# Kernel optimization log

Hardware: AMD Instinct MI355X
Metric: run time of the kernel (lower is better)

The kernel has to match this reference:

```python
import jax, jax.numpy as jnp
import numpy as np

B, C, H, W = 32, 512, 32, 32
N = H * W            # seq_len = 1024
HEADS = 8
DH = C // HEADS      # 64
K = 256              # linformer low-rank
EPS = 1e-5


def setup_inputs() -> dict:
    key = jax.random.key(0)
    ks = jax.random.split(key, 10)
    s = 0.02
    return {
        "x": jax.random.normal(ks[0], (B, C, H, W), dtype=jnp.float32),
        "pos": jax.random.normal(ks[1], (1, N, C), dtype=jnp.float32),
        "ln_g": jnp.ones((C,), dtype=jnp.float32),
        "ln_b": jnp.zeros((C,), dtype=jnp.float32),
        "Wq": jax.random.normal(ks[2], (C, C), dtype=jnp.float32) * s,
        "Wk": jax.random.normal(ks[3], (C, C), dtype=jnp.float32) * s,
        "Wv": jax.random.normal(ks[4], (C, C), dtype=jnp.float32) * s,
        "proj_k": jax.random.normal(ks[5], (N, K), dtype=jnp.float32) * s,
        "proj_v": jax.random.normal(ks[6], (N, K), dtype=jnp.float32) * s,
        "Wo": jax.random.normal(ks[7], (C, C), dtype=jnp.float32) * s,
        "bo": jnp.zeros((C,), dtype=jnp.float32),
    }


def reference(x, pos, ln_g, ln_b, Wq, Wk, Wv, proj_k, proj_v, Wo, bo):
    b, c, h, w = x.shape
    n = h * w
    # b c h w -> b (h w) c
    xf = x.reshape(b, c, n).transpose(0, 2, 1) + pos
    # LayerNorm (biased variance, eps=1e-5) + ReLU; dropout = identity (eval)
    mu = xf.mean(-1, keepdims=True)
    var = jnp.var(xf, axis=-1, keepdims=True)
    y = (xf - mu) * jax.lax.rsqrt(var + EPS) * ln_g + ln_b
    y = jax.nn.relu(y)
    # Linformer self-attention
    q = y @ Wq                                   # [b,n,c]
    k_ = jnp.einsum('bnd,nk->bkd', y @ Wk, proj_k)  # [b,K,c]
    v_ = jnp.einsum('bnd,nk->bkd', y @ Wv, proj_v)  # [b,K,c]
    q = q.reshape(b, n, HEADS, DH)
    k_ = k_.reshape(b, K, HEADS, DH)
    v_ = v_.reshape(b, K, HEADS, DH)
    dots = jnp.einsum('bnhd,bkhd->bhnk', q, k_) * (DH ** -0.5)
    attn = jax.nn.softmax(dots, axis=-1)
    out = jnp.einsum('bhnk,bkhd->bnhd', attn, v_).reshape(b, n, c)
    out = out @ Wo + bo
    # residual with (x + pos), then back to b c h w
    out = out + xf
    return out.transpose(0, 2, 1).reshape(b, c, h, w)
```

## Files before the change

kernel.cpp:

```cpp
#include <hip/hip_runtime.h>
#include <hip/hip_bf16.h>
#include <cstdint>

#define BB  32
#define CC  512
#define NN  1024
#define HH  8
#define DHH 64
#define KR  256

using f32x4  = __attribute__((ext_vector_type(4))) float;
using f32x16 = __attribute__((ext_vector_type(16))) float;
using bf16x8 = __attribute__((ext_vector_type(8))) __bf16;
using u32x4  = __attribute__((ext_vector_type(4))) unsigned int;

__device__ __forceinline__ unsigned short f2bf(float f) {
  unsigned int u = __float_as_uint(f);
  u += 0x7fffu + ((u >> 16) & 1u);
  return (unsigned short)(u >> 16);
}

__device__ __forceinline__ float bf2f(unsigned short u) {
  return __uint_as_float(((unsigned int)u) << 16);
}

__device__ __forceinline__ unsigned int pknat(float a, float b) {
  unsigned short ua = __builtin_bit_cast(unsigned short, (__bf16)a);
  unsigned short ub = __builtin_bit_cast(unsigned short, (__bf16)b);
  return (unsigned int)ua | ((unsigned int)ub << 16);
}

__device__ __forceinline__ void gload16(const void* gsrc, void* ldst) {
  __builtin_amdgcn_global_load_lds(
      (const __attribute__((address_space(1))) unsigned int*)gsrc,
      (__attribute__((address_space(3))) unsigned int*)ldst, 16, 0, 0);
}

__global__ __launch_bounds__(256) void transcvt_all(
    const float* __restrict__ w0, const float* __restrict__ w1,
    const float* __restrict__ w2, const float* __restrict__ w3,
    const float* __restrict__ p0, const float* __restrict__ p1,
    const float* __restrict__ pos,
    unsigned short* __restrict__ d0, unsigned short* __restrict__ d1,
    unsigned short* __restrict__ d2, unsigned short* __restrict__ d3,
    unsigned short* __restrict__ e0, unsigned short* __restrict__ e1,
    float* __restrict__ posT) {
  const int m = blockIdx.y;
  int idx = blockIdx.x * 256 + threadIdx.x;
  if (m == 6) {
    #pragma unroll
    for (int h = 0; h < 2; ++h) {
      int e = idx + h * 262144;
      int c = e >> 10, n = e & 1023;
      posT[e] = pos[(size_t)n * CC + c];
    }
    return;
  }
  const float* src = m==0?w0:m==1?w1:m==2?w2:m==3?w3:m==4?p0:p1;
  unsigned short* dst = m==0?d0:m==1?d1:m==2?d2:m==3?d3:m==4?e0:e1;
  if (m < 4) {
    int dr = idx & 511;
    int dc = idx >> 9;
    dst[idx] = f2bf(src[(size_t)dr * 512 + dc]);
  } else {
    int n = idx & 1023, kk = idx >> 10;
    dst[idx] = f2bf(src[(size_t)n * 256 + kk]);
  }
}

__global__ __launch_bounds__(1024) void ln_relu_kernel(
    const float* __restrict__ x, const float* __restrict__ posT,
    const float* __restrict__ g, const float* __restrict__ bta,
    unsigned short* __restrict__ y, unsigned short* __restrict__ yT) {
  __shared__ unsigned short tile[512][68];
  __shared__ float smp[16][16][8];
  __shared__ float smu[64], srs[64];
  const int b = blockIdx.y, n0 = blockIdx.x * 64;
  const int tid = threadIdx.x;
  const int wv = tid >> 6, ln_ = tid & 63;
  const int q = tid & 15;
  const int rr = tid >> 4;
  const int t4 = q * 4;
  const float* xb = x    + (size_t)b * CC * NN + n0;
  const float* pb = posT + n0;

  float s[4] = {0.f,0.f,0.f,0.f}, s2[4] = {0.f,0.f,0.f,0.f};
  #pragma unroll
  for (int half = 0; half < 2; ++half) {
    float4 xv[4], pv[4];
    #pragma unroll
    for (int i = 0; i < 4; ++i) {
      const int c = (half * 4 + i) * 64 + rr;
      xv[i] = *reinterpret_cast<const float4*>(&xb[(size_t)c * NN + t4]);
      pv[i] = *reinterpret_cast<const float4*>(&pb[(size_t)c * NN + t4]);
    }
    #pragma unroll
    for (int i = 0; i < 4; ++i) {
      const int c = (half * 4 + i) * 64 + rr;
      float f0 = xv[i].x + pv[i].x, f1 = xv[i].y + pv[i].y;
      float f2 = xv[i].z + pv[i].z, f3 = xv[i].w + pv[i].w;
      s[0] += f0; s2[0] += f0 * f0;
      s[1] += f1; s2[1] += f1 * f1;
      s[2] += f2; s2[2] += f2 * f2;
      s[3] += f3; s2[3] += f3 * f3;
      uint2 w; w.x = pknat(f0, f1); w.y = pknat(f2, f3);
      *reinterpret_cast<uint2*>(&tile[c][t4]) = w;
    }
  }
  #pragma unroll
  for (int d = 16; d < 64; d <<= 1)
    #pragma unroll
    for (int k = 0; k < 4; ++k) {
      s[k]  += __shfl_xor(s[k],  d, 64);
      s2[k] += __shfl_xor(s2[k], d, 64);
    }
  if (ln_ < 16) {
    #pragma unroll
    for (int k = 0; k < 4; ++k) {
      smp[wv][ln_][k]     = s[k];
      smp[wv][ln_][k + 4] = s2[k];
    }
  }
  __syncthreads();

  if (tid < 64) {
    const int qq = tid >> 2, k = tid & 3;
    float ss = 0.f, ss2 = 0.f;
    #pragma unroll
    for (int w = 0; w < 16; ++w) { ss += smp[w][qq][k]; ss2 += smp[w][qq][k + 4]; }
    float mu = ss * (1.f / 512.f);
    float var = ss2 * (1.f / 512.f) - mu * mu;
    smu[tid] = mu;
    srs[tid] = rsqrtf(var + 1e-5f);
  }
  __syncthreads();

  {
    const int cq = tid & 127;
    const int c0 = cq * 4;
    const float4 gv = *reinterpret_cast<const float4*>(&g[c0]);
    const float4 bv = *reinterpret_cast<const float4*>(&bta[c0]);
    #pragma unroll
    for (int it = 0; it < 8; ++it) {
      const int tok = it * 8 + (tid >> 7);
      const float mu = smu[tok], rs = srs[tok];
      float o0 = (bf2f(tile[c0 + 0][tok]) - mu) * rs * gv.x + bv.x;
      float o1 = (bf2f(tile[c0 + 1][tok]) - mu) * rs * gv.y + bv.y;
      float o2 = (bf2f(tile[c0 + 2][tok]) - mu) * rs * gv.z + bv.z;
      float o3 = (bf2f(tile[c0 + 3][tok]) - mu) * rs * gv.w + bv.w;
      o0 = o0 > 0.f ? o0 : 0.f;
      o1 = o1 > 0.f ? o1 : 0.f;
      o2 = o2 > 0.f ? o2 : 0.f;
      o3 = o3 > 0.f ? o3 : 0.f;
      unsigned short b0 = f2bf(o0), b1 = f2bf(o1), b2 = f2bf(o2), b3 = f2bf(o3);
      uint2 u; u.x = (unsigned int)b0 | ((unsigned int)b1 << 16);
      u.y = (unsigned int)b2 | ((unsigned int)b3 << 16);
      *reinterpret_cast<uint2*>(&y[((size_t)b * NN + n0 + tok) * CC + c0]) = u;
      tile[c0 + 0][tok] = b0; tile[c0 + 1][tok] = b1;
      tile[c0 + 2][tok] = b2; tile[c0 + 3][tok] = b3;
    }
  }
  __syncthreads();

  {
    const int c = tid & 511, hf = tid >> 9;
    const int toff = hf * 32;
    unsigned short* ytb = yT + (size_t)b * CC * NN + (size_t)c * NN + n0 + toff;
    #pragma unroll
    for (int v4 = 0; v4 < 4; ++v4) {
      uint2 a0 = *reinterpret_cast<const uint2*>(&tile[c][toff + v4 * 8]);
      uint2 a1 = *reinterpret_cast<const uint2*>(&tile[c][toff + v4 * 8 + 4]);
      uint4 w; w.x = a0.x; w.y = a0.y; w.z = a1.x; w.w = a1.y;
      *reinterpret_cast<uint4*>(&ytb[v4 * 8]) = w;
    }
  }
}

template <int MODE>
__global__ __launch_bounds__(256) void gemm_tn(
    const unsigned short* __restrict__ A, int lda, long long strideA,
    const unsigned short* __restrict__ Bt, int ldb, long long strideB,
    unsigned short* __restrict__ Cb, long long strideC,
    unsigned short* __restrict__ Cb2, long long strideC2,
    int Nn, int Kk, int TB,
    const float* __restrict__ xres, const float* __restrict__ posT,
    const float* __restrict__ bias, float* __restrict__ outF) {
  __shared__ __align__(16) unsigned short sh[24576];
  unsigned short* aL = sh;
  unsigned short* bL = sh + 12288;
  const int zb = blockIdx.z;
  int sel = 0, mb;
  if (MODE == 3) {
    sel = blockIdx.y >> 1;
    mb = ((blockIdx.y & 1) + sel * 2) * 128;
    if (sel == 1) Bt += (size_t)512 * 512;
  } else {
    mb = blockIdx.y * 128;
  }
  const int nb = blockIdx.x * 128;
  A  += (size_t)strideA * zb;
  Bt += (size_t)strideB * zb;
  Cb += (size_t)strideC * zb;
  if (MODE == 3) Cb2 += (size_t)strideC2 * zb;
  const int tid  = threadIdx.x;
  const int lane = tid & 63;
  const int wave = tid >> 6;
  const int wm = (wave >> 1) * 64, wn = (wave & 1) * 64;
  const int sr  = lane >> 2;
  const int scw = lane & 3;
  f32x4 acc[4][4] = {};

  auto stage = [&](int buf, int k0) {
    #pragma unroll
    for (int i = 0; i < 2; ++i) {
      int rbase = wave * 32 + i * 16;
      int row = rbase + sr;
      int ca = scw ^ ((row ^ (row >> 2)) & 3);
      gload16(&A [(size_t)(mb + row) * lda + k0 + ca * 8], &aL[buf * 4096 + rbase * 32]);
      gload16(&Bt[(size_t)(nb + row) * ldb + k0 + ca * 8], &bL[buf * 4096 + rbase * 32]);
    }
  };

  const int nt = Kk >> 5;
  stage(0, 0);
  stage(1, 32);
  asm volatile("s_waitcnt vmcnt(4)" ::: "memory");
  __builtin_amdgcn_s_barrier();
  __builtin_amdgcn_sched_barrier(0);

  int cbuf = 0;
  for (int t = 0; t < nt; ++t) {
    if (t + 2 < nt) stage(cbuf == 0 ? 2 : cbuf - 1, (t + 2) << 5);

    bf16x8 af[4], bfv[4];
    const int kc = lane >> 4;
    #pragma unroll
    for (int i = 0; i < 4; ++i) {
      int ra = wm + i * 16 + (lane & 15);
      int rb = wn + i * 16 + (lane & 15);
      af[i]  = *reinterpret_cast<const bf16x8*>(&aL[cbuf * 4096 + ra * 32 + (kc ^ ((ra ^ (ra >> 2)) & 3)) * 8]);
      bfv[i] = *reinterpret_cast<const bf16x8*>(&bL[cbuf * 4096 + rb * 32 + (kc ^ ((rb ^ (rb >> 2)) & 3)) * 8]);
    }
    #pragma unroll
    for (int i = 0; i < 4; ++i)
      #pragma unroll
      for (int j = 0; j < 4; ++j)
        acc[i][j] = __builtin_amdgcn_mfma_f32_16x16x32_bf16(af[i], bfv[j], acc[i][j], 0, 0, 0);

    if (t + 2 < nt)      { asm volatile("s_waitcnt vmcnt(4)" ::: "memory"); }
    else if (t + 1 < nt) { asm volatile("s_waitcnt vmcnt(0)" ::: "memory"); }
    if (t + 1 < nt) {
      __builtin_amdgcn_s_barrier();
      __builtin_amdgcn_sched_barrier(0);
    }
    cbuf = (cbuf == 2) ? 0 : cbuf + 1;
  }

  if (MODE == 2) {
    float* Ct = reinterpret_cast<float*>(sh);
    const int halfsel = wave >> 1;
    const int t0base = nb & 1023;
    const int bcell = nb >> 10;
    #pragma unroll
    for (int half = 0; half < 2; ++half) {
      __syncthreads();
      if (halfsel == half) {
        #pragma unroll
        for (int i = 0; i < 4; ++i) {
          int rloc = i * 16 + ((lane >> 4) << 2);
          #pragma unroll
          for (int j = 0; j < 4; ++j) {
            int cl = wn + j * 16 + (lane & 15);
            #pragma unroll
            for (int t = 0; t < 4; ++t)
              Ct[(rloc + t) * 132 + cl] = acc[i][j][t];
          }
        }
      }
      __syncthreads();
      #pragma unroll
      for (int p8 = 0; p8 < 8; ++p8) {
        int e = p8 * 256 + tid;
        int r = e >> 5, f4 = (e & 31) * 4;
        int c = mb + half * 64 + r;
        size_t base = ((size_t)bcell * CC + c) * NN + t0base + f4;
        float4 cv = *reinterpret_cast<const float4*>(&Ct[r * 132 + f4]);
        float4 xv = *reinterpret_cast<const float4*>(&xres[base]);
        float4 pv = *reinterpret_cast<const float4*>(&posT[(size_t)c * NN + t0base + f4]);
        float bc = bias[c];
        float4 ov;
        ov.x = cv.x + xv.x + pv.x + bc;
        ov.y = cv.y + xv.y + pv.y + bc;
        ov.z = cv.z + xv.z + pv.z + bc;
        ov.w = cv.w + xv.w + pv.w + bc;
        *reinterpret_cast<float4*>(&outF[base]) = ov;
      }
    }
  } else {
    const bool transp = (MODE == 1) || (MODE == 3 && sel == 1);
    auto Ct = (unsigned short (*)[136])sh;
    __syncthreads();
    #pragma unroll
    for (int i = 0; i < 4; ++i) {
      const int r0 = wm + i * 16 + ((lane >> 4) << 2);
      #pragma unroll
      for (int j = 0; j < 4; ++j) {
        const int cl = wn + j * 16 + (lane & 15);
        #pragma unroll
        for (int t = 0; t < 4; ++t) {
          if (!transp) Ct[r0 + t][cl] = f2bf(acc[i][j][t]);
          else         Ct[cl][r0 + t] = f2bf(acc[i][j][t]);
        }
      }
    }
    __syncthreads();
    const int rr = tid >> 4, ch = tid & 15;
    #pragma unroll
    for (int it = 0; it < 8; ++it) {
      const int r = it * 16 + rr;
      uint4 v = *reinterpret_cast<const uint4*>(&Ct[r][ch * 8]);
      if (!transp)
        *reinterpret_cast<uint4*>(&Cb[(size_t)(mb + r) * Nn + nb + ch * 8]) = v;
      else if (MODE == 1)
        *reinterpret_cast<uint4*>(&Cb[(size_t)(nb + r) * TB + mb + ch * 8]) = v;
      else
        *reinterpret_cast<uint4*>(&Cb2[(size_t)(nb + r) * TB + (mb - 256) + ch * 8]) = v;
    }
  }
}

__global__ __launch_bounds__(256, 2) void attn_kernel(
    const unsigned short* __restrict__ q,
    const unsigned short* __restrict__ kB,
    const unsigned short* __restrict__ vT,
    unsigned short* __restrict__ O) {
  __shared__ __align__(16) unsigned short smem[32768];
  const int wgid = blockIdx.x;
  const int grp  = wgid & 255;
  const int tg   = wgid >> 8;
  const int h = grp & 7, b = grp >> 3;
  const int wave = threadIdx.x >> 6, lane = threadIdx.x & 63;
  const int t32 = lane & 31, g2 = lane >> 5;
  const int tokb = tg * 128 + wave * 32;

  const unsigned short* qp = q + ((size_t)(b * NN + tokb + t32)) * CC + h * DHH + g2 * 8;
  bf16x8 qf[4];
  #pragma unroll
  for (int st = 0; st < 4; ++st)
    qf[st] = *reinterpret_cast<const bf16x8*>(qp + (size_t)st * 16);

  {
    const unsigned short* kb = kB + ((size_t)b * KR) * CC + h * DHH;
    const int r0w = wave * 64;
    #pragma unroll
    for (int i = 0; i < 8; ++i) {
      int row = r0w + i * 8 + (lane >> 3);
      int sc  = (lane & 7) ^ (row & 7);
      gload16(kb + (size_t)row * CC + sc * 8, &smem[(r0w + i * 8) * 64]);
    }
    const unsigned short* vb = vT + ((size_t)b * CC + h * DHH) * KR;
    const int v0w = wave * 16;
    #pragma unroll
    for (int i = 0; i < 8; ++i) {
      int row = v0w + i * 2 + (lane >> 5);
      int sc  = (lane & 31) ^ (row & 7);
      gload16(vb + (size_t)row * KR + sc * 8, &smem[16384 + (v0w + i * 2) * 256]);
    }
  }
  __syncthreads();

  f32x16 s8[8] = {};
  #pragma unroll
  for (int t8 = 0; t8 < 8; ++t8) {
    const int row = t8 * 32 + t32;
    #pragma unroll
    for (int st = 0; st < 4; ++st) {
      int ch = (2 * st + g2) ^ (row & 7);
      bf16x8 kf = *reinterpret_cast<const bf16x8*>(&smem[row * 64 + ch * 8]);
      s8[t8] = __builtin_amdgcn_mfma_f32_32x32x16_bf16(kf, qf[st], s8[t8], 0, 0, 0);
    }
  }

  float m = -1e30f;
  #pragma unroll
  for (int t8 = 0; t8 < 8; ++t8)
    #pragma unroll
    for (int r = 0; r < 16; ++r) m = fmaxf(m, s8[t8][r]);
  m = fmaxf(m, __shfl_xor(m, 32));
  const float cexp = 0.125f * 1.44269504088896f;
  float ls = 0.f;
  #pragma unroll
  for (int t8 = 0; t8 < 8; ++t8)
    #pragma unroll
    for (int r = 0; r < 16; ++r) {
      float p = __builtin_amdgcn_exp2f((s8[t8][r] - m) * cexp);
      s8[t8][r] = p;
      ls += p;
    }
  ls += __shfl_xor(ls, 32);
  float rinv = __builtin_amdgcn_rcpf(ls);

  f32x16 o0 = {}, o1 = {};
  #pragma unroll
  for (int t8 = 0; t8 < 8; ++t8) {
    unsigned int pkd[8];
    #pragma unroll
    for (int qq = 0; qq < 4; ++qq) {
      pkd[qq * 2 + 0] = pknat(s8[t8][4 * qq + 0], s8[t8][4 * qq + 1]);
      pkd[qq * 2 + 1] = pknat(s8[t8][4 * qq + 2], s8[t8][4 * qq + 3]);
    }
    #pragma unroll
    for (int a = 0; a < 2; ++a) {
      const int ks = t8 * 2 + a;
      unsigned int xe0 = pkd[4 * a + 0], xe1 = pkd[4 * a + 1];
      unsigned int xo0 = pkd[4 * a + 2], xo1 = pkd[4 * a + 3];
      unsigned int d0 = g2 ? __shfl_xor(xo0, 32) : xe0;
      unsigned int d1 = g2 ? __shfl_xor(xo1, 32) : xe1;
      unsigned int d2 = g2 ? xo0 : __shfl_xor(xe0, 32);
      unsigned int d3 = g2 ? xo1 : __shfl_xor(xe1, 32);
      u32x4 pv_ = {d0, d1, d2, d3};
      bf16x8 pa = __builtin_bit_cast(bf16x8, pv_);
      #pragma unroll
      for (int dt = 0; dt < 2; ++dt) {
        int row = dt * 32 + t32;
        int ch = (2 * ks + g2) ^ (row & 7);
        bf16x8 bv = *reinterpret_cast<const bf16x8*>(&smem[16384 + row * 256 + ch * 8]);
        if (dt == 0) o0 = __builtin_amdgcn_mfma_f32_32x32x16_bf16(pa, bv, o0, 0, 0, 0);
        else         o1 = __builtin_amdgcn_mfma_f32_32x32x16_bf16(pa, bv, o1, 0, 0, 0);
      }
    }
  }

  unsigned short* Ob = O + ((size_t)(b * NN + tokb)) * CC + h * DHH;
  #pragma unroll
  for (int r = 0; r < 16; ++r) {
    int tl = (r & 3) + 8 * (r >> 2) + 4 * g2;
    float rs = __shfl(rinv, tl);
    Ob[(size_t)tl * CC + t32]      = f2bf(o0[r] * rs);
    Ob[(size_t)tl * CC + 32 + t32] = f2bf(o1[r] * rs);
  }
}

extern "C" void kernel_launch(void* const* d_in, const int* in_sizes, int n_in,
                              void* d_out, int out_size, void* d_ws, size_t ws_size,
                              hipStream_t stream) {
  const float* x    = (const float*)d_in[0];
  const float* pos  = (const float*)d_in[1];
  const float* ln_g = (const float*)d_in[2];
  const float* ln_b = (const float*)d_in[3];
  const float* Wq   = (const float*)d_in[4];
  const float* Wk   = (const float*)d_in[5];
  const float* Wv   = (const float*)d_in[6];
  const float* pk   = (const float*)d_in[7];
  const float* pv   = (const float*)d_in[8];
  const float* Wo   = (const float*)d_in[9];
  const float* bo   = (const float*)d_in[10];
  float* out = (float*)d_out;

  unsigned short* ws = (unsigned short*)d_ws;
  size_t off = 0;
  auto alloc = [&](size_t elems) { unsigned short* p = ws + off; off += elems; return p; };
  unsigned short* WqT     = alloc(512 * 512);
  unsigned short* WkT     = alloc(512 * 512);
  unsigned short* WvT     = alloc(512 * 512);
  unsigned short* WoT     = alloc(512 * 512);
  unsigned short* projcat = alloc((size_t)512 * 1024);
  float*          posTb   = (float*)alloc((size_t)512 * 1024 * 2);
  unsigned short* yB      = alloc((size_t)32768 * 512);
  unsigned short* yT      = alloc((size_t)32 * 512 * 1024);
  unsigned short* qB      = alloc((size_t)32768 * 512);
  unsigned short* zB      = alloc((size_t)32 * 512 * 512);
  unsigned short* kBuf    = alloc((size_t)32 * 256 * 512);
  unsigned short* vTB     = alloc((size_t)32 * 512 * 256);
  unsigned short* OB      = alloc((size_t)32768 * 512);

  transcvt_all<<<dim3(1024, 7), 256, 0, stream>>>(
      Wq, Wk, Wv, Wo, pk, pv, pos,
      WqT, WkT, WvT, WoT, projcat, projcat + (size_t)256 * 1024, posTb);

  ln_relu_kernel<<<dim3(16, 32), 1024, 0, stream>>>(x, posTb, ln_g, ln_b, yB, yT);

  gemm_tn<0><<<dim3(4, 256), 256, 0, stream>>>(
      yB, 512, 0, WqT, 512, 0, qB, 0, nullptr, 0,
      512, 512, 0, nullptr, nullptr, nullptr, nullptr);

  gemm_tn<0><<<dim3(4, 4, 32), 256, 0, stream>>>(
      projcat, 1024, 0, yT, 1024, (long long)512 * 1024, zB, (long long)512 * 512,
      nullptr, 0, 512, 1024, 0, nullptr, nullptr, nullptr, nullptr);

  gemm_tn<3><<<dim3(4, 4, 32), 256, 0, stream>>>(
      zB, 512, (long long)512 * 512, WkT, 512, 0, kBuf, (long long)256 * 512,
      vTB, (long long)512 * 256, 512, 512, 256, nullptr, nullptr, nullptr, nullptr);

  attn_kernel<<<dim3(2048, 1, 1), 256, 0, stream>>>(qB, kBuf, vTB, OB);

  gemm_tn<2><<<dim3(256, 4), 256, 0, stream>>>(
      WoT, 512, 0, OB, 512, 0, nullptr, 0, nullptr, 0,
      32768, 512, 0, x, posTb, bo, out);
}
```

Measured before the change: 202.1 us.

## Keep LN inputs in registers, write y via LDS transpose, prefetch residual in epilogue

```diff
diff --git a/kernel.cpp b/kernel.cpp
--- a/kernel.cpp
+++ b/kernel.cpp
@@ -80,31 +80,30 @@
   const int wv = tid >> 6, ln_ = tid & 63;
   const int q = tid & 15;
   const int rr = tid >> 4;
-  const int t4 = q * 4;
-  const float* xb = x    + (size_t)b * CC * NN + n0;
-  const float* pb = posT + n0;
-
+  const float* xb = x    + (size_t)b * CC * NN + n0 + q * 4;
+  const float* pb = posT + n0 + q * 4;
+
+  float4 xf[8];
   float s[4] = {0.f,0.f,0.f,0.f}, s2[4] = {0.f,0.f,0.f,0.f};
   #pragma unroll
-  for (int half = 0; half < 2; ++half) {
+  for (int hh = 0; hh < 2; ++hh) {
     float4 xv[4], pv[4];
     #pragma unroll
     for (int i = 0; i < 4; ++i) {
-      const int c = (half * 4 + i) * 64 + rr;
-      xv[i] = *reinterpret_cast<const float4*>(&xb[(size_t)c * NN + t4]);
-      pv[i] = *reinterpret_cast<const float4*>(&pb[(size_t)c * NN + t4]);
+      const int c = rr + (hh * 4 + i) * 64;
+      xv[i] = *reinterpret_cast<const float4*>(&xb[(size_t)c * NN]);
+      pv[i] = *reinterpret_cast<const float4*>(&pb[(size_t)c * NN]);
     }
     #pragma unroll
     for (int i = 0; i < 4; ++i) {
-      const int c = (half * 4 + i) * 64 + rr;
-      float f0 = xv[i].x + pv[i].x, f1 = xv[i].y + pv[i].y;
-      float f2 = xv[i].z + pv[i].z, f3 = xv[i].w + pv[i].w;
-      s[0] += f0; s2[0] += f0 * f0;
-      s[1] += f1; s2[1] += f1 * f1;
-      s[2] += f2; s2[2] += f2 * f2;
-      s[3] += f3; s2[3] += f3 * f3;
-      uint2 w; w.x = pknat(f0, f1); w.y = pknat(f2, f3);
-      *reinterpret_cast<uint2*>(&tile[c][t4]) = w;
+      float4 f;
+      f.x = xv[i].x + pv[i].x; f.y = xv[i].y + pv[i].y;
+      f.z = xv[i].z + pv[i].z; f.w = xv[i].w + pv[i].w;
+      s[0] += f.x; s2[0] += f.x * f.x;
+      s[1] += f.y; s2[1] += f.y * f.y;
+      s[2] += f.z; s2[2] += f.z * f.z;
+      s[3] += f.w; s2[3] += f.w * f.w;
+      xf[hh * 4 + i] = f;
     }
   }
   #pragma unroll
@@ -136,31 +135,44 @@
   __syncthreads();
 
   {
-    const int cq = tid & 127;
-    const int c0 = cq * 4;
-    const float4 gv = *reinterpret_cast<const float4*>(&g[c0]);
-    const float4 bv = *reinterpret_cast<const float4*>(&bta[c0]);
-    #pragma unroll
-    for (int it = 0; it < 8; ++it) {
-      const int tok = it * 8 + (tid >> 7);
-      const float mu = smu[tok], rs = srs[tok];
-      float o0 = (bf2f(tile[c0 + 0][tok]) - mu) * rs * gv.x + bv.x;
-      float o1 = (bf2f(tile[c0 + 1][tok]) - mu) * rs * gv.y + bv.y;
-      float o2 = (bf2f(tile[c0 + 2][tok]) - mu) * rs * gv.z + bv.z;
-      float o3 = (bf2f(tile[c0 + 3][tok]) - mu) * rs * gv.w + bv.w;
-      o0 = o0 > 0.f ? o0 : 0.f;
-      o1 = o1 > 0.f ? o1 : 0.f;
-      o2 = o2 > 0.f ? o2 : 0.f;
-      o3 = o3 > 0.f ? o3 : 0.f;
-      unsigned short b0 = f2bf(o0), b1 = f2bf(o1), b2 = f2bf(o2), b3 = f2bf(o3);
-      uint2 u; u.x = (unsigned int)b0 | ((unsigned int)b1 << 16);
-      u.y = (unsigned int)b2 | ((unsigned int)b3 << 16);
-      *reinterpret_cast<uint2*>(&y[((size_t)b * NN + n0 + tok) * CC + c0]) = u;
-      tile[c0 + 0][tok] = b0; tile[c0 + 1][tok] = b1;
-      tile[c0 + 2][tok] = b2; tile[c0 + 3][tok] = b3;
+    const float mu0 = smu[q * 4 + 0], rs0 = srs[q * 4 + 0];
+    const float mu1 = smu[q * 4 + 1], rs1 = srs[q * 4 + 1];
+    const float mu2 = smu[q * 4 + 2], rs2 = srs[q * 4 + 2];
+    const float mu3 = smu[q * 4 + 3], rs3 = srs[q * 4 + 3];
+    #pragma unroll
+    for (int i = 0; i < 8; ++i) {
+      const int c = rr + i * 64;
+      const float gg = g[c], bb = bta[c];
+      float o0 = (xf[i].x - mu0) * rs0 * gg + bb; o0 = o0 > 0.f ? o0 : 0.f;
+      float o1 = (xf[i].y - mu1) * rs1 * gg + bb; o1 = o1 > 0.f ? o1 : 0.f;
+      float o2 = (xf[i].z - mu2) * rs2 * gg + bb; o2 = o2 > 0.f ? o2 : 0.f;
+      float o3 = (xf[i].w - mu3) * rs3 * gg + bb; o3 = o3 > 0.f ? o3 : 0.f;
+      uint2 u; u.x = pknat(o0, o1); u.y = pknat(o2, o3);
+      *reinterpret_cast<uint2*>(&tile[c][q * 4]) = u;
     }
   }
   __syncthreads();
+
+  {
+    const int tok = tid >> 4, seg = tid & 15;
+    const int c0 = seg * 32;
+    unsigned int pk16[16];
+    #pragma unroll
+    for (int cc = 0; cc < 32; cc += 2) {
+      const int ccr = (cc + seg * 2) & 31;
+      unsigned short v0 = tile[c0 + ccr][tok];
+      unsigned short v1 = tile[c0 + ccr + 1][tok];
+      pk16[ccr >> 1] = (unsigned int)v0 | ((unsigned int)v1 << 16);
+    }
+    unsigned short* yb = y + ((size_t)b * NN + n0 + tok) * CC + c0;
+    #pragma unroll
+    for (int v4 = 0; v4 < 4; ++v4) {
+      uint4 w;
+      w.x = pk16[v4 * 4 + 0]; w.y = pk16[v4 * 4 + 1];
+      w.z = pk16[v4 * 4 + 2]; w.w = pk16[v4 * 4 + 3];
+      *reinterpret_cast<uint4*>(&yb[v4 * 8]) = w;
+    }
+  }
 
   {
     const int c = tid & 511, hf = tid >> 9;
@@ -261,6 +273,17 @@
     const int halfsel = wave >> 1;
     const int t0base = nb & 1023;
     const int bcell = nb >> 10;
+    float4 xr[16];
+    #pragma unroll
+    for (int half = 0; half < 2; ++half)
+      #pragma unroll
+      for (int p8 = 0; p8 < 8; ++p8) {
+        int e = p8 * 256 + tid;
+        int r = e >> 5, f4 = (e & 31) * 4;
+        int c = mb + half * 64 + r;
+        xr[half * 8 + p8] = *reinterpret_cast<const float4*>(
+            &xres[((size_t)bcell * CC + c) * NN + t0base + f4]);
+      }
     #pragma unroll
     for (int half = 0; half < 2; ++half) {
       __syncthreads();
@@ -285,7 +308,7 @@
         int c = mb + half * 64 + r;
         size_t base = ((size_t)bcell * CC + c) * NN + t0base + f4;
         float4 cv = *reinterpret_cast<const float4*>(&Ct[r * 132 + f4]);
-        float4 xv = *reinterpret_cast<const float4*>(&xres[base]);
+        float4 xv = xr[half * 8 + p8];
         float4 pv = *reinterpret_cast<const float4*>(&posT[(size_t)c * NN + t0base + f4]);
         float bc = bias[c];
         float4 ov;
```

New measurement: 209.3 us. 3.6% more time.
